# Optimization experiments

Hardware: AMD Instinct MI355X
Metric: run time of the kernel (lower is better)

Reference implementation:

```python
import jax, jax.numpy as jnp
import numpy as np

N, E = 30000, 480000
D_IN, D_HID = 128, 256
NODE_CLS, EDGE_CLS, POLAR = 5, 2, 6
EPS = 1e-5

def layer_norm(x, g, b):
    mu = jnp.mean(x, axis=-1, keepdims=True)
    var = jnp.mean((x - mu) ** 2, axis=-1, keepdims=True)
    return g * (x - mu) / jnp.sqrt(var + EPS) + b

def sage_pool(h, src, dst, Wp, bp, Ws, bs, Wn, n_nodes):
    # DGL SAGEConv aggregator_type='pool': m = relu(fc_pool(h_src)); max over in-edges
    m = jax.nn.relu(h @ Wp + bp)              # [N, d_in]
    agg = jax.ops.segment_max(m[src], dst, num_segments=n_nodes)  # [N, d_in], -inf if no in-edges
    deg = jax.ops.segment_sum(jnp.ones((src.shape[0],), jnp.float32), dst, num_segments=n_nodes)
    h_neigh = jnp.where(deg[:, None] > 0, agg, 0.0)
    out = h @ Ws + bs + h_neigh @ Wn          # fc_self + fc_neigh
    return jax.nn.relu(out)                   # activation=F.relu

def setup_inputs() -> dict:
    key = jax.random.key(0)
    ks = jax.random.split(key, 24)
    p = lambda k, shape, fan: jax.random.normal(k, shape, jnp.float32) / np.sqrt(fan)
    return {
        "h": jax.random.normal(ks[0], (N, D_IN), jnp.float32),
        "efeat": jax.random.normal(ks[1], (E, POLAR), jnp.float32),
        "src": jax.random.randint(ks[2], (E,), 0, N, jnp.int32),
        "dst": jax.random.randint(ks[3], (E,), 0, N, jnp.int32),
        # encoder SAGEConv(128->256)
        "enc_Wpool": p(ks[4], (D_IN, D_IN), D_IN), "enc_bpool": jnp.zeros((D_IN,), jnp.float32),
        "enc_Wself": p(ks[5], (D_IN, D_HID), D_IN), "enc_bself": jnp.zeros((D_HID,), jnp.float32),
        "enc_Wneigh": p(ks[6], (D_IN, D_HID), D_IN),
        # node_pred: Linear(256,5) + LayerNorm(5)
        "np_W": p(ks[7], (D_HID, NODE_CLS), D_HID), "np_b": jnp.zeros((NODE_CLS,), jnp.float32),
        "np_g": jnp.ones((NODE_CLS,), jnp.float32), "np_beta": jnp.zeros((NODE_CLS,), jnp.float32),
        # edge predictor: Linear(528,256) + LN(256) + Linear(256,2)
        "ep_W1": p(ks[8], (2 * D_HID + 2 * NODE_CLS + POLAR, D_HID), 2 * D_HID + 16),
        "ep_b1": jnp.zeros((D_HID,), jnp.float32),
        "ep_g": jnp.ones((D_HID,), jnp.float32), "ep_beta": jnp.zeros((D_HID,), jnp.float32),
        "ep_W2": p(ks[9], (D_HID, EDGE_CLS), D_HID), "ep_b2": jnp.zeros((EDGE_CLS,), jnp.float32),
        # decoder SAGEConv(256->128)
        "dec_Wpool": p(ks[10], (D_HID, D_HID), D_HID), "dec_bpool": jnp.zeros((D_HID,), jnp.float32),
        "dec_Wself": p(ks[11], (D_HID, D_IN), D_HID), "dec_bself": jnp.zeros((D_IN,), jnp.float32),
        "dec_Wneigh": p(ks[12], (D_HID, D_IN), D_HID),
    }

def reference(h, efeat, src, dst,
              enc_Wpool, enc_bpool, enc_Wself, enc_bself, enc_Wneigh,
              np_W, np_b, np_g, np_beta,
              ep_W1, ep_b1, ep_g, ep_beta, ep_W2, ep_b2,
              dec_Wpool, dec_bpool, dec_Wself, dec_bself, dec_Wneigh):
    # encoder (drop_rate == 0 path)
    h1 = sage_pool(h, src, dst, enc_Wpool, enc_bpool, enc_Wself, enc_bself, enc_Wneigh, N)
    # node head
    node_pred = layer_norm(h1 @ np_W + np_b, np_g, np_beta)  # [N, 5]
    # edge head: gather-concat-MLP per edge
    cls_sm = jax.nn.softmax(node_pred, axis=1)               # softmax once, gather per edge
    x = jnp.concatenate([h1[src], cls_sm[src], efeat, h1[dst], cls_sm[dst]], axis=1)  # [E, 528]
    x = jax.nn.relu(layer_norm(x @ ep_W1 + ep_b1, ep_g, ep_beta))
    edges_pred = x @ ep_W2 + ep_b2                           # dropout is identity in eval
    # decoder (uses original graph, input h1)
    h2 = sage_pool(h1, src, dst, dec_Wpool, dec_bpool, dec_Wself, dec_bself, dec_Wneigh, N)
    return (node_pred, edges_pred, h2)
```

## Files before the change

kernel.cpp:

```cpp
#include <hip/hip_runtime.h>

typedef unsigned short u16;
typedef unsigned int u32;
typedef __bf16 bf16_t;
typedef bf16_t bf16x8 __attribute__((ext_vector_type(8)));
typedef float f32x4 __attribute__((ext_vector_type(4)));
typedef float f32x2 __attribute__((ext_vector_type(2)));

#define N_NODES 30000
#define N_EDGES 480000

static __device__ __forceinline__ float b2f(u16 u) {
  return __uint_as_float(((u32)u) << 16);
}
static __device__ __forceinline__ float b2f_lo(u32 w) {
  return __uint_as_float(w << 16);
}
static __device__ __forceinline__ float b2f_hi(u32 w) {
  return __uint_as_float(w & 0xffff0000u);
}
static __device__ __forceinline__ u16 f2b(float f) {
  u32 x = __float_as_uint(f);
  u32 r = (x + 0x7fffu + ((x >> 16) & 1u)) >> 16;
  return (u16)r;
}

__global__ __launch_bounds__(256) void init_sniff_deg(const u16* __restrict__ h,
                                                      int* __restrict__ flag,
                                                      int* __restrict__ deg) {
  int i = blockIdx.x * 256 + threadIdx.x;
  if (i < N_NODES) deg[i] = 0;
  if (blockIdx.x == 0) {
    int t = threadIdx.x;
    int bad = 0;
#pragma unroll
    for (int j = 0; j < 4; j++) {
      u32 e = ((u32)h[t * 4 + j] >> 7) & 0xFFu;
      if (e >= 0x8Eu) bad = 1;
    }
    int r = __syncthreads_or(bad);
    if (t == 0) *flag = r ? 1 : 0;
  }
}

struct ConvDesc { const void* s; u16* d; int n; int off; };
struct ConvTab { ConvDesc e[20]; int total; };

__global__ __launch_bounds__(256) void conv_all(
    const int* __restrict__ dstE, int* __restrict__ deg,
    const void* __restrict__ hsrc, u16* __restrict__ c_h,
    const void* __restrict__ efsrc, u16* __restrict__ c_ef,
    ConvTab tab, const int* __restrict__ flag) {
  int b = blockIdx.x;
  const int t = threadIdx.x;
  if (b < 1875) {
    int e = b * 256 + t;
    if (e < N_EDGES) atomicAdd(&deg[dstE[e]], 1);
    return;
  }
  b -= 1875;
  const int f = *flag;
  if (b < 3750) {
    int i = b * 256 + t;
    if (f) {
      float4 v = ((const float4*)hsrc)[i];
      uint2 o;
      o.x = (u32)f2b(v.x) | ((u32)f2b(v.y) << 16);
      o.y = (u32)f2b(v.z) | ((u32)f2b(v.w) << 16);
      ((uint2*)c_h)[i] = o;
    } else {
      ((uint2*)c_h)[i] = ((const uint2*)hsrc)[i];
    }
    return;
  }
  b -= 3750;
  if (b < 2813) {
    int i = b * 256 + t;
    if (i < 720000) {
      if (f) {
        float4 v = ((const float4*)efsrc)[i];
        uint2 o;
        o.x = (u32)f2b(v.x) | ((u32)f2b(v.y) << 16);
        o.y = (u32)f2b(v.z) | ((u32)f2b(v.w) << 16);
        ((uint2*)c_ef)[i] = o;
      } else {
        ((uint2*)c_ef)[i] = ((const uint2*)efsrc)[i];
      }
    }
    return;
  }
  b -= 2813;
  int i = b * 256 + t;
  if (i >= tab.total) return;
#pragma unroll 1
  for (int a = 0; a < 20; a++) {
    int j = i - tab.e[a].off;
    if (j >= 0 && j < tab.e[a].n) {
      if (f) tab.e[a].d[j] = f2b(((const float*)tab.e[a].s)[j]);
      else tab.e[a].d[j] = ((const u16*)tab.e[a].s)[j];
      return;
    }
  }
}

__global__ __launch_bounds__(1024) void scan_off(const int* __restrict__ deg,
                                                 int* __restrict__ off,
                                                 int* __restrict__ cursor, int n) {
  __shared__ int carry;
  __shared__ int wsum[16];
  int t = threadIdx.x, lane = t & 63, wv = t >> 6;
  if (t == 0) { carry = 0; off[0] = 0; }
  __syncthreads();
  for (int base = 0; base < n; base += 1024) {
    int v = (base + t < n) ? deg[base + t] : 0;
    int x = v;
#pragma unroll
    for (int d = 1; d < 64; d <<= 1) {
      int y = __shfl_up(x, d, 64);
      if (lane >= d) x += y;
    }
    if (lane == 63) wsum[wv] = x;
    __syncthreads();
    int wadd = 0;
    for (int w = 0; w < wv; w++) wadd += wsum[w];
    int incl = x + wadd + carry;
    if (base + t < n) { off[base + t + 1] = incl; cursor[base + t] = incl - v; }
    __syncthreads();
    if (t == 1023) carry = incl;
    __syncthreads();
  }
}

__global__ __launch_bounds__(256) void fill_csr(const int* __restrict__ src,
                                                const int* __restrict__ dst,
                                                int* __restrict__ cursor,
                                                int* __restrict__ esrc, int nE) {
  int e = blockIdx.x * 256 + threadIdx.x;
  if (e >= nE) return;
  int p = atomicAdd(&cursor[dst[e]], 1);
  esrc[p] = src[e];
}

__global__ __launch_bounds__(256) void agg128(const u16* __restrict__ m,
                                              const int* __restrict__ esrc,
                                              const int* __restrict__ off,
                                              u16* __restrict__ out) {
  int wv = threadIdx.x >> 6, lane = threadIdx.x & 63;
  int qd = lane >> 4, l = lane & 15;
  int n = blockIdx.x * 16 + wv * 4 + qd;
  if (n >= N_NODES) return;
  int i = off[n], s1 = off[n + 1];
  u32 a0 = 0, a1 = 0, a2 = 0, a3 = 0, a4 = 0, a5 = 0, a6 = 0, a7 = 0;
  for (; i + 1 < s1; i += 2) {
    int e0 = esrc[i], e1 = esrc[i + 1];
    uint4 r0 = *(const uint4*)(m + (size_t)e0 * 128 + l * 8);
    uint4 r1 = *(const uint4*)(m + (size_t)e1 * 128 + l * 8);
    a0 = max(a0, r0.x & 0xffffu); a1 = max(a1, r0.x >> 16);
    a2 = max(a2, r0.y & 0xffffu); a3 = max(a3, r0.y >> 16);
    a4 = max(a4, r0.z & 0xffffu); a5 = max(a5, r0.z >> 16);
    a6 = max(a6, r0.w & 0xffffu); a7 = max(a7, r0.w >> 16);
    a0 = max(a0, r1.x & 0xffffu); a1 = max(a1, r1.x >> 16);
    a2 = max(a2, r1.y & 0xffffu); a3 = max(a3, r1.y >> 16);
    a4 = max(a4, r1.z & 0xffffu); a5 = max(a5, r1.z >> 16);
    a6 = max(a6, r1.w & 0xffffu); a7 = max(a7, r1.w >> 16);
  }
  if (i < s1) {
    uint4 r0 = *(const uint4*)(m + (size_t)esrc[i] * 128 + l * 8);
    a0 = max(a0, r0.x & 0xffffu); a1 = max(a1, r0.x >> 16);
    a2 = max(a2, r0.y & 0xffffu); a3 = max(a3, r0.y >> 16);
    a4 = max(a4, r0.z & 0xffffu); a5 = max(a5, r0.z >> 16);
    a6 = max(a6, r0.w & 0xffffu); a7 = max(a7, r0.w >> 16);
  }
  uint4 w;
  w.x = a0 | (a1 << 16); w.y = a2 | (a3 << 16);
  w.z = a4 | (a5 << 16); w.w = a6 | (a7 << 16);
  *(uint4*)(out + (size_t)n * 128 + l * 8) = w;
}

__global__ __launch_bounds__(256) void agg256(const u16* __restrict__ m,
                                              const int* __restrict__ esrc,
                                              const int* __restrict__ off,
                                              u16* __restrict__ out) {
  int wv = threadIdx.x >> 6, lane = threadIdx.x & 63;
  int half = lane >> 5, l = lane & 31;
  int n = blockIdx.x * 8 + wv * 2 + half;
  if (n >= N_NODES) return;
  int i = off[n], s1 = off[n + 1];
  u32 a0 = 0, a1 = 0, a2 = 0, a3 = 0, a4 = 0, a5 = 0, a6 = 0, a7 = 0;
  for (; i + 1 < s1; i += 2) {
    int e0 = esrc[i], e1 = esrc[i + 1];
    uint4 r0 = *(const uint4*)(m + (size_t)e0 * 256 + l * 8);
    uint4 r1 = *(const uint4*)(m + (size_t)e1 * 256 + l * 8);
    a0 = max(a0, r0.x & 0xffffu); a1 = max(a1, r0.x >> 16);
    a2 = max(a2, r0.y & 0xffffu); a3 = max(a3, r0.y >> 16);
    a4 = max(a4, r0.z & 0xffffu); a5 = max(a5, r0.z >> 16);
    a6 = max(a6, r0.w & 0xffffu); a7 = max(a7, r0.w >> 16);
    a0 = max(a0, r1.x & 0xffffu); a1 = max(a1, r1.x >> 16);
    a2 = max(a2, r1.y & 0xffffu); a3 = max(a3, r1.y >> 16);
    a4 = max(a4, r1.z & 0xffffu); a5 = max(a5, r1.z >> 16);
    a6 = max(a6, r1.w & 0xffffu); a7 = max(a7, r1.w >> 16);
  }
  if (i < s1) {
    uint4 r0 = *(const uint4*)(m + (size_t)esrc[i] * 256 + l * 8);
    a0 = max(a0, r0.x & 0xffffu); a1 = max(a1, r0.x >> 16);
    a2 = max(a2, r0.y & 0xffffu); a3 = max(a3, r0.y >> 16);
    a4 = max(a4, r0.z & 0xffffu); a5 = max(a5, r0.z >> 16);
    a6 = max(a6, r0.w & 0xffffu); a7 = max(a7, r0.w >> 16);
  }
  uint4 w;
  w.x = a0 | (a1 << 16); w.y = a2 | (a3 << 16);
  w.z = a4 | (a5 << 16); w.w = a6 | (a7 << 16);
  *(uint4*)(out + (size_t)n * 256 + l * 8) = w;
}

__global__ __launch_bounds__(256) void prep_weights(
    const u16* __restrict__ encWp, const u16* __restrict__ encWs, const u16* __restrict__ encWn,
    const u16* __restrict__ decWp, const u16* __restrict__ decWs, const u16* __restrict__ decWn,
    const u16* __restrict__ epW1, const u16* __restrict__ epb1,
    u16* __restrict__ wt_encpool, u16* __restrict__ wt_enc,
    u16* __restrict__ wt_decpool, u16* __restrict__ wt_dec,
    u16* __restrict__ wt_UV, u16* __restrict__ b512, float* __restrict__ swsum) {
  int b = blockIdx.x;
  const int t = threadIdx.x;
  if (b < 64) {
    int idx = b * 256 + t; int k = idx >> 7, n = idx & 127;
    wt_encpool[n * 128 + k] = encWp[k * 128 + n]; return;
  }
  b -= 64;
  if (b < 128) {
    int idx = b * 256 + t; int k = idx >> 8, n = idx & 255;
    wt_enc[n * 256 + k] = encWs[k * 256 + n]; return;
  }
  b -= 128;
  if (b < 128) {
    int idx = b * 256 + t; int k = idx >> 8, n = idx & 255;
    wt_enc[n * 256 + 128 + k] = encWn[k * 256 + n]; return;
  }
  b -= 128;
  if (b < 256) {
    int idx = b * 256 + t; int k = idx >> 8, n = idx & 255;
    wt_decpool[n * 256 + k] = decWp[k * 256 + n]; return;
  }
  b -= 256;
  if (b < 128) {
    int idx = b * 256 + t; int k = idx >> 7, n = idx & 127;
    wt_dec[n * 512 + k] = decWs[k * 128 + n]; return;
  }
  b -= 128;
  if (b < 128) {
    int idx = b * 256 + t; int k = idx >> 7, n = idx & 127;
    wt_dec[n * 512 + 256 + k] = decWn[k * 128 + n]; return;
  }
  b -= 128;
  if (b < 512) {
    int n = b, n2 = n & 255, base = (n >= 256) ? 267 : 0;
    for (int kp = t; kp < 288; kp += 256) {
      u16 v = (kp < 261) ? epW1[(size_t)(base + kp) * 256 + n2] : (u16)0;
      wt_UV[(size_t)n * 288 + kp] = v;
    }
    return;
  }
  b -= 512;
  if (b < 2) {
    int i = b * 256 + t;
    b512[i] = (i < 256) ? epb1[i] : (u16)0; return;
  }
  int k = t >> 5, l32 = t & 31;
  if (k < 6) {
    uint4 v = *(const uint4*)(epW1 + (size_t)(261 + k) * 256 + l32 * 8);
    float s = b2f_lo(v.x) + b2f_hi(v.x) + b2f_lo(v.y) + b2f_hi(v.y) +
              b2f_lo(v.z) + b2f_hi(v.z) + b2f_lo(v.w) + b2f_hi(v.w);
#pragma unroll
    for (int m = 1; m < 32; m <<= 1) s += __shfl_xor(s, m, 64);
    if (l32 == 0) swsum[k] = s;
  }
}

__global__ __launch_bounds__(256) void gemm_mfma(
    const u16* __restrict__ A0, const u16* __restrict__ A1, int K0, int K1,
    const u16* __restrict__ Bt, const u16* __restrict__ bias, int do_relu,
    u16* __restrict__ C, float* __restrict__ Cf, const int* __restrict__ flag,
    int M, int Nld) {
  __shared__ __align__(16) u16 As[128 * 40];
  __shared__ __align__(16) u16 Bs[128 * 40];
  const int t = threadIdx.x;
  const int lane = t & 63, wv = t >> 6;
  const int wm = wv & 1, wn = wv >> 1;
  const int r = lane & 15, q = lane >> 4;
  const int bm = blockIdx.x, bn = blockIdx.y;
  const int Ktot = K0 + K1;
  const bool usef = (Cf != nullptr) && (*flag != 0);

  f32x4 acc[4][4];
#pragma unroll
  for (int i = 0; i < 4; i++)
#pragma unroll
    for (int j = 0; j < 4; j++) acc[i][j] = (f32x4){0.f, 0.f, 0.f, 0.f};

  for (int kc = 0; kc < Ktot; kc += 32) {
#pragma unroll
    for (int h = 0; h < 2; h++) {
      int idx = t + h * 256;
      int rr = idx >> 2, qq = idx & 3;
      int rowg = bm * 128 + rr;
      uint4 av = make_uint4(0, 0, 0, 0);
      if (rowg < M) {
        const u16* p = (kc < K0) ? (A0 + (size_t)rowg * K0 + kc)
                                 : (A1 + (size_t)rowg * K1 + (kc - K0));
        av = *(const uint4*)(p + qq * 8);
      }
      *(uint4*)&As[rr * 40 + qq * 8] = av;
      int ng = bn * 128 + rr;
      uint4 bv = *(const uint4*)(Bt + (size_t)ng * Ktot + kc + qq * 8);
      *(uint4*)&Bs[rr * 40 + qq * 8] = bv;
    }
    __syncthreads();
    bf16x8 af[4], bfm[4];
#pragma unroll
    for (int mi = 0; mi < 4; mi++)
      af[mi] = *(const bf16x8*)&As[(wm * 64 + mi * 16 + r) * 40 + q * 8];
#pragma unroll
    for (int ni = 0; ni < 4; ni++)
      bfm[ni] = *(const bf16x8*)&Bs[(wn * 64 + ni * 16 + r) * 40 + q * 8];
#pragma unroll
    for (int mi = 0; mi < 4; mi++)
#pragma unroll
      for (int ni = 0; ni < 4; ni++)
        acc[mi][ni] = __builtin_amdgcn_mfma_f32_16x16x32_bf16(af[mi], bfm[ni], acc[mi][ni], 0, 0, 0);
    __syncthreads();
  }

  float bv[4];
#pragma unroll
  for (int ni = 0; ni < 4; ni++)
    bv[ni] = bias ? b2f(bias[bn * 128 + wn * 64 + ni * 16 + r]) : 0.f;
#pragma unroll
  for (int mi = 0; mi < 4; mi++) {
#pragma unroll
    for (int i = 0; i < 4; i++) {
      int rowg = bm * 128 + wm * 64 + mi * 16 + q * 4 + i;
      if (rowg >= M) continue;
#pragma unroll
      for (int ni = 0; ni < 4; ni++) {
        int colg = bn * 128 + wn * 64 + ni * 16 + r;
        float v = acc[mi][ni][i] + bv[ni];
        if (do_relu) v = v > 0.f ? v : 0.f;
        if (usef) Cf[(size_t)rowg * Nld + colg] = v;
        else C[(size_t)rowg * Nld + colg] = f2b(v);
      }
    }
  }
}

__global__ __launch_bounds__(256) void node_head(
    const u16* __restrict__ h1, const u16* __restrict__ W, const u16* __restrict__ b,
    const u16* __restrict__ g, const u16* __restrict__ beta,
    u16* __restrict__ outN, float* __restrict__ outNf, const int* __restrict__ flag,
    u16* __restrict__ smOut) {
  __shared__ float Wl[256 * 5];
  __shared__ float bl[5], gl[5], betal[5];
  int t = threadIdx.x;
#pragma unroll
  for (int c = 0; c < 5; c++) Wl[t * 5 + c] = b2f(W[t * 5 + c]);
  if (t < 5) { bl[t] = b2f(b[t]); gl[t] = b2f(g[t]); betal[t] = b2f(beta[t]); }
  __syncthreads();
  int n = blockIdx.x * 256 + t;
  if (n >= N_NODES) return;
  const bool usef = (*flag != 0);
  float acc[5] = {0.f, 0.f, 0.f, 0.f, 0.f};
  const u16* hp = h1 + (size_t)n * 256;
  for (int k8 = 0; k8 < 32; k8++) {
    uint4 v = *(const uint4*)(hp + k8 * 8);
    u32 wds[4] = {v.x, v.y, v.z, v.w};
#pragma unroll
    for (int h = 0; h < 4; h++) {
      float x0 = b2f_lo(wds[h]), x1 = b2f_hi(wds[h]);
      int k = k8 * 8 + h * 2;
#pragma unroll
      for (int c = 0; c < 5; c++)
        acc[c] += x0 * Wl[k * 5 + c] + x1 * Wl[(k + 1) * 5 + c];
    }
  }
  float x[5], mu = 0.f;
#pragma unroll
  for (int c = 0; c < 5; c++) { x[c] = acc[c] + bl[c]; mu += x[c]; }
  mu *= 0.2f;
  float var = 0.f;
#pragma unroll
  for (int c = 0; c < 5; c++) { float d = x[c] - mu; var += d * d; }
  var *= 0.2f;
  float rstd = rsqrtf(fmaxf(var, 0.f) + 1e-5f);
  float v5[5], mx = -1e30f;
#pragma unroll
  for (int c = 0; c < 5; c++) {
    v5[c] = gl[c] * (x[c] - mu) * rstd + betal[c];
    if (usef) outNf[(size_t)n * 5 + c] = v5[c];
    else outN[(size_t)n * 5 + c] = f2b(v5[c]);
    mx = fmaxf(mx, v5[c]);
  }
  float s = 0.f, ex[5];
#pragma unroll
  for (int c = 0; c < 5; c++) { ex[c] = __expf(v5[c] - mx); s += ex[c]; }
  float inv = 1.f / s;
  u16 row[32];
#pragma unroll
  for (int c = 0; c < 5; c++) row[c] = f2b(ex[c] * inv);
#pragma unroll
  for (int c = 5; c < 32; c++) row[c] = 0;
#pragma unroll
  for (int c = 0; c < 4; c++)
    *(uint4*)(smOut + (size_t)n * 32 + c * 8) = *(const uint4*)&row[c * 8];
}

__global__ __launch_bounds__(256) void rowsum_uv(const u16* __restrict__ UV,
                                                 float2* __restrict__ Srow) {
  int wv = threadIdx.x >> 6, lane = threadIdx.x & 63;
  int n = blockIdx.x * 4 + wv;
  if (n >= N_NODES) return;
  uint4 v = *(const uint4*)(UV + (size_t)n * 512 + lane * 8);
  float s = b2f_lo(v.x) + b2f_hi(v.x) + b2f_lo(v.y) + b2f_hi(v.y) +
            b2f_lo(v.z) + b2f_hi(v.z) + b2f_lo(v.w) + b2f_hi(v.w);
#pragma unroll
  for (int m = 1; m < 32; m <<= 1) s += __shfl_xor(s, m, 64);
  if (lane == 0) Srow[n].x = s;
  if (lane == 32) Srow[n].y = s;
}

__global__ __launch_bounds__(256) void edge_mean(
    const int* __restrict__ src, const int* __restrict__ dst,
    const u16* __restrict__ ef, const float2* __restrict__ Srow,
    const float* __restrict__ swsum, uint4* __restrict__ recs) {
  int p = blockIdx.x * 256 + threadIdx.x;
  if (p >= 240000) return;
  int e = p * 2;
  int s0 = src[e], s1 = src[e + 1];
  int d0 = dst[e], d1 = dst[e + 1];
  const u32* efp = (const u32*)(ef + (size_t)e * 6);
  u32 f0 = efp[0], f1 = efp[1], f2 = efp[2], f3 = efp[3], f4 = efp[4], f5 = efp[5];
  float xa[6] = {b2f_lo(f0), b2f_hi(f0), b2f_lo(f1), b2f_hi(f1), b2f_lo(f2), b2f_hi(f2)};
  float xb[6] = {b2f_lo(f3), b2f_hi(f3), b2f_lo(f4), b2f_hi(f4), b2f_lo(f5), b2f_hi(f5)};
  float sw[6];
#pragma unroll
  for (int k = 0; k < 6; k++) sw[k] = swsum[k];
  float m0 = Srow[s0].x + Srow[d0].y;
  float m1 = Srow[s1].x + Srow[d1].y;
#pragma unroll
  for (int k = 0; k < 6; k++) { m0 += xa[k] * sw[k]; m1 += xb[k] * sw[k]; }
  m0 *= (1.f / 256.f);
  m1 *= (1.f / 256.f);
  uint4 ra, rb, rc;
  ra.x = (u32)s0; ra.y = (u32)d0; ra.z = (u32)s1; ra.w = (u32)d1;
  rb.x = __float_as_uint(m0); rb.y = __float_as_uint(m1); rb.z = f0; rb.w = f1;
  rc.x = f2; rc.y = f3; rc.z = f4; rc.w = f5;
  recs[(size_t)p * 3 + 0] = ra;
  recs[(size_t)p * 3 + 1] = rb;
  recs[(size_t)p * 3 + 2] = rc;
}

__global__ __launch_bounds__(256) void edge_pt(
    const u16* __restrict__ UV, const uint4* __restrict__ recs,
    const u16* __restrict__ w1raw,
    const u16* __restrict__ g, const u16* __restrict__ beta,
    const u16* __restrict__ w2, const u16* __restrict__ b2,
    u16* __restrict__ outE, float* __restrict__ outEf, const int* __restrict__ flag) {
  const int t = threadIdx.x;
  const int lane = t & 63, wv = t >> 6;
  const int c0 = lane * 4;
  const int grp = (lane >> 4) & 3;
  f32x2 wefA[6], wefB[6];
#pragma unroll
  for (int k = 0; k < 6; k++) {
    u32 wa = *(const u32*)(w1raw + (size_t)(261 + k) * 256 + c0);
    u32 wb = *(const u32*)(w1raw + (size_t)(261 + k) * 256 + c0 + 2);
    wefA[k] = (f32x2){b2f_lo(wa), b2f_hi(wa)};
    wefB[k] = (f32x2){b2f_lo(wb), b2f_hi(wb)};
  }
  f32x2 glA = (f32x2){b2f(g[c0]), b2f(g[c0 + 1])};
  f32x2 glB = (f32x2){b2f(g[c0 + 2]), b2f(g[c0 + 3])};
  f32x2 blA = (f32x2){b2f(beta[c0]), b2f(beta[c0 + 1])};
  f32x2 blB = (f32x2){b2f(beta[c0 + 2]), b2f(beta[c0 + 3])};
  float w20[4], w21[4];
#pragma unroll
  for (int j = 0; j < 4; j++) {
    w20[j] = b2f(w2[(c0 + j) * 2]); w21[j] = b2f(w2[(c0 + j) * 2 + 1]);
  }
  const float b20 = b2f(b2[0]), b21 = b2f(b2[1]);
  const float bsel = (grp & 1) ? b21 : b20;
  const bool usef = (*flag != 0);
  const f32x2 zero2 = (f32x2){0.f, 0.f};

  const int pb = __builtin_amdgcn_readfirstlane((blockIdx.x * 4 + wv) * 16);
  const uint4* rp = recs + (size_t)pb * 3;
  uint4 ra = rp[0], rb = rp[1], rc = rp[2];
#pragma unroll 1
  for (int it = 0; it < 16; ++it) {
    const int e = (pb + it) * 2;
    uint4 ca = ra, cb = rb, cc = rc;
    ra = rp[3 * it + 3]; rb = rp[3 * it + 4]; rc = rp[3 * it + 5];
    const int s0 = (int)ca.x, d0 = (int)ca.y, s1 = (int)ca.z, d1 = (int)ca.w;
    const float ma = __uint_as_float(cb.x), mb = __uint_as_float(cb.y);
    float xa[6] = {b2f_lo(cb.z), b2f_hi(cb.z), b2f_lo(cb.w), b2f_hi(cb.w),
                   b2f_lo(cc.x), b2f_hi(cc.x)};
    float xb[6] = {b2f_lo(cc.y), b2f_hi(cc.y), b2f_lo(cc.z), b2f_hi(cc.z),
                   b2f_lo(cc.w), b2f_hi(cc.w)};
    uint2 ua = *(const uint2*)(UV + ((size_t)(u32)s0 << 9) + c0);
    uint2 va = *(const uint2*)(UV + ((size_t)(u32)d0 << 9) + 256 + c0);
    uint2 ub = *(const uint2*)(UV + ((size_t)(u32)s1 << 9) + c0);
    uint2 vb = *(const uint2*)(UV + ((size_t)(u32)d1 << 9) + 256 + c0);

    f32x2 yaA = (f32x2){b2f_lo(ua.x), b2f_hi(ua.x)} + (f32x2){b2f_lo(va.x), b2f_hi(va.x)};
    f32x2 yaB = (f32x2){b2f_lo(ua.y), b2f_hi(ua.y)} + (f32x2){b2f_lo(va.y), b2f_hi(va.y)};
    f32x2 ybA = (f32x2){b2f_lo(ub.x), b2f_hi(ub.x)} + (f32x2){b2f_lo(vb.x), b2f_hi(vb.x)};
    f32x2 ybB = (f32x2){b2f_lo(ub.y), b2f_hi(ub.y)} + (f32x2){b2f_lo(vb.y), b2f_hi(vb.y)};
#pragma unroll
    for (int k = 0; k < 6; k++) {
      yaA += xa[k] * wefA[k];
      yaB += xa[k] * wefB[k];
      ybA += xb[k] * wefA[k];
      ybB += xb[k] * wefB[k];
    }
    float pqa = yaA.x * yaA.x;
    pqa += yaA.y * yaA.y; pqa += yaB.x * yaB.x; pqa += yaB.y * yaB.y;
    float pqb = ybA.x * ybA.x;
    pqb += ybA.y * ybA.y; pqb += ybB.x * ybB.x; pqb += ybB.y * ybB.y;
    pqa += __shfl_xor(pqa, 32, 64);
    pqb += __shfl_xor(pqb, 32, 64);
    float z = (lane < 32) ? pqa : pqb;
#pragma unroll
    for (int m = 16; m >= 1; m >>= 1) z += __shfl_xor(z, m, 64);
    float zz = __shfl_xor(z, 32, 64);
    float pqa_t = (lane < 32) ? z : zz;
    float pqb_t = (lane < 32) ? zz : z;
    float rsa = rsqrtf(fmaxf(pqa_t * (1.f / 256.f) - ma * ma, 0.f) + 1e-5f);
    float rsb = rsqrtf(fmaxf(pqb_t * (1.f / 256.f) - mb * mb, 0.f) + 1e-5f);
    f32x2 nAa = __builtin_elementwise_max((yaA - ma) * rsa * glA + blA, zero2);
    f32x2 nAb = __builtin_elementwise_max((yaB - ma) * rsa * glB + blB, zero2);
    f32x2 nBa = __builtin_elementwise_max((ybA - mb) * rsb * glA + blA, zero2);
    f32x2 nBb = __builtin_elementwise_max((ybB - mb) * rsb * glB + blB, zero2);
    float p0a = nAa.x * w20[0], p1a = nAa.x * w21[0];
    p0a += nAa.y * w20[1]; p1a += nAa.y * w21[1];
    p0a += nAb.x * w20[2]; p1a += nAb.x * w21[2];
    p0a += nAb.y * w20[3]; p1a += nAb.y * w21[3];
    float p0b = nBa.x * w20[0], p1b = nBa.x * w21[0];
    p0b += nBa.y * w20[1]; p1b += nBa.y * w21[1];
    p0b += nBb.x * w20[2]; p1b += nBb.x * w21[2];
    p0b += nBb.y * w20[3]; p1b += nBb.y * w21[3];
    p0a += __shfl_xor(p0a, 32, 64); p1a += __shfl_xor(p1a, 32, 64);
    p0b += __shfl_xor(p0b, 32, 64); p1b += __shfl_xor(p1b, 32, 64);
    p0a += __shfl_xor(p0a, 16, 64); p1a += __shfl_xor(p1a, 16, 64);
    p0b += __shfl_xor(p0b, 16, 64); p1b += __shfl_xor(p1b, 16, 64);
    float w = (grp & 2) ? ((grp & 1) ? p1b : p0b) : ((grp & 1) ? p1a : p0a);
#pragma unroll
    for (int m = 8; m >= 1; m >>= 1) w += __shfl_xor(w, m, 64);
    if ((lane & 15) == 0) {
      float val = w + bsel;
      size_t oi = (size_t)e * 2 + grp;
      if (usef) outEf[oi] = val;
      else outE[oi] = f2b(val);
    }
  }
}

extern "C" void kernel_launch(void* const* d_in, const int* in_sizes, int n_in,
                              void* d_out, int out_size, void* d_ws, size_t ws_size,
                              hipStream_t stream) {
  char* wp = (char*)d_ws;
  auto alloc = [&](size_t bytes) -> char* {
    char* p = wp; wp += (bytes + 255) & ~(size_t)255; return p;
  };
  int* flag       = (int*)alloc(256);
  u16* c_h        = (u16*)alloc((size_t)N_NODES * 128 * 2);
  u16* c_ef       = (u16*)alloc((size_t)N_EDGES * 6 * 2);
  static const int pidx[20] = {4,5,6,7,8, 9,10,11,12, 13,14,15,16,17,18, 19,20,21,22,23};
  static const int pn[20]   = {16384,128,32768,256,32768, 1280,5,5,5,
                               135168,256,256,256,512,2, 65536,256,32768,128,32768};
  u16* cp[20];
  for (int a = 0; a < 20; a++) cp[a] = (u16*)alloc((size_t)pn[a] * 2);

  u16* wt_encpool = (u16*)alloc(128 * 128 * 2);
  u16* wt_enc     = (u16*)alloc(256 * 256 * 2);
  u16* wt_decpool = (u16*)alloc(256 * 256 * 2);
  u16* wt_dec     = (u16*)alloc(128 * 512 * 2);
  u16* wt_UV      = (u16*)alloc(512 * 288 * 2);
  u16* b512       = (u16*)alloc(512 * 2);
  float2* Srow    = (float2*)alloc((size_t)N_NODES * 8);
  float* swsum_b  = (float*)alloc(64);
  u16* m_buf      = (u16*)alloc((size_t)N_NODES * 256 * 2);
  u16* aggb       = (u16*)alloc((size_t)N_NODES * 256 * 2);
  u16* UVbuf      = m_buf;
  u16* h1b        = (u16*)alloc((size_t)N_NODES * 256 * 2);
  u16* smb32      = (u16*)alloc((size_t)N_NODES * 32 * 2);
  int* deg        = (int*)alloc((size_t)N_NODES * 4);
  int* off        = (int*)alloc((size_t)(N_NODES + 1) * 4);
  int* cursor     = (int*)alloc((size_t)N_NODES * 4);
  int* esrc       = (int*)alloc((size_t)N_EDGES * 4);
  uint4* recs     = (uint4*)alloc(((size_t)240000 * 3 + 8) * 16);

  const int* src = (const int*)d_in[2];
  const int* dst = (const int*)d_in[3];

  u16* outN = (u16*)d_out;
  u16* outE = outN + (size_t)N_NODES * 5;
  u16* outH = outN + 1110000;
  float* outNf = (float*)d_out;
  float* outEf = outNf + (size_t)N_NODES * 5;
  float* outHf = outNf + 1110000;

  init_sniff_deg<<<118, 256, 0, stream>>>((const u16*)d_in[0], flag, deg);
  ConvTab tab;
  int off_a = 0;
  for (int a = 0; a < 20; a++) {
    tab.e[a].s = d_in[pidx[a]]; tab.e[a].d = cp[a]; tab.e[a].n = pn[a]; tab.e[a].off = off_a;
    off_a += pn[a];
  }
  tab.total = off_a;
  int conv_blocks = 1875 + 3750 + 2813 + (off_a + 255) / 256;
  conv_all<<<conv_blocks, 256, 0, stream>>>(dst, deg, d_in[0], c_h, d_in[1], c_ef, tab, flag);

  const u16 *enc_Wpool = cp[0], *enc_bpool = cp[1], *enc_Wself = cp[2], *enc_bself = cp[3],
            *enc_Wneigh = cp[4], *np_W = cp[5], *np_b = cp[6], *np_g = cp[7], *np_beta = cp[8],
            *ep_W1 = cp[9], *ep_b1 = cp[10], *ep_g = cp[11], *ep_beta = cp[12],
            *ep_W2 = cp[13], *ep_b2 = cp[14], *dec_Wpool = cp[15], *dec_bpool = cp[16],
            *dec_Wself = cp[17], *dec_bself = cp[18], *dec_Wneigh = cp[19];

  scan_off<<<1, 1024, 0, stream>>>(deg, off, cursor, N_NODES);
  fill_csr<<<1875, 256, 0, stream>>>(src, dst, cursor, esrc, N_EDGES);

  prep_weights<<<1347, 256, 0, stream>>>(enc_Wpool, enc_Wself, enc_Wneigh,
                                         dec_Wpool, dec_Wself, dec_Wneigh,
                                         ep_W1, ep_b1,
                                         wt_encpool, wt_enc, wt_decpool, wt_dec,
                                         wt_UV, b512, swsum_b);

  gemm_mfma<<<dim3(235, 1), 256, 0, stream>>>(c_h, nullptr, 128, 0, wt_encpool,
                                              enc_bpool, 1, m_buf, nullptr, flag, N_NODES, 128);
  agg128<<<1875, 256, 0, stream>>>(m_buf, esrc, off, aggb);
  gemm_mfma<<<dim3(235, 2), 256, 0, stream>>>(c_h, aggb, 128, 128, wt_enc,
                                              enc_bself, 1, h1b, nullptr, flag, N_NODES, 256);
  node_head<<<118, 256, 0, stream>>>(h1b, np_W, np_b, np_g, np_beta, outN, outNf, flag, smb32);
  gemm_mfma<<<dim3(235, 4), 256, 0, stream>>>(h1b, smb32, 256, 32, wt_UV,
                                              b512, 0, UVbuf, nullptr, flag, N_NODES, 512);
  rowsum_uv<<<7500, 256, 0, stream>>>(UVbuf, Srow);
  edge_mean<<<938, 256, 0, stream>>>(src, dst, c_ef, Srow, swsum_b, recs);
  edge_pt<<<3750, 256, 0, stream>>>(UVbuf, recs, ep_W1, ep_g, ep_beta, ep_W2, ep_b2,
                                    outE, outEf, flag);
  gemm_mfma<<<dim3(235, 2), 256, 0, stream>>>(h1b, nullptr, 256, 0, wt_decpool,
                                              dec_bpool, 1, m_buf, nullptr, flag, N_NODES, 256);
  agg256<<<3750, 256, 0, stream>>>(m_buf, esrc, off, aggb);
  gemm_mfma<<<dim3(235, 1), 256, 0, stream>>>(h1b, aggb, 256, 256, wt_dec,
                                              dec_bself, 1, outH, outHf, flag, N_NODES, 128);
}
```

Before: 461.1 us.

## Software-pipeline edge UV gathers, unroll aggregation loops, and single-pass offset scan

Result: no change. 467.4 us (+1.4%).

```diff
diff --git a/kernel.cpp b/kernel.cpp
--- a/kernel.cpp
+++ b/kernel.cpp
@@ -106,28 +106,40 @@
 __global__ __launch_bounds__(1024) void scan_off(const int* __restrict__ deg,
                                                  int* __restrict__ off,
                                                  int* __restrict__ cursor, int n) {
-  __shared__ int carry;
   __shared__ int wsum[16];
-  int t = threadIdx.x, lane = t & 63, wv = t >> 6;
-  if (t == 0) { carry = 0; off[0] = 0; }
+  const int t = threadIdx.x, lane = t & 63, wv = t >> 6;
+  const int CH = 30;
+  int base = t * CH;
+  int v[CH];
+  int s = 0;
+#pragma unroll
+  for (int j = 0; j < CH; j++) {
+    int idx = base + j;
+    int d = (idx < n) ? deg[idx] : 0;
+    v[j] = s;
+    s += d;
+  }
+  int x = s;
+#pragma unroll
+  for (int d = 1; d < 64; d <<= 1) {
+    int y = __shfl_up(x, d, 64);
+    if (lane >= d) x += y;
+  }
+  if (lane == 63) wsum[wv] = x;
   __syncthreads();
-  for (int base = 0; base < n; base += 1024) {
-    int v = (base + t < n) ? deg[base + t] : 0;
-    int x = v;
-#pragma unroll
-    for (int d = 1; d < 64; d <<= 1) {
-      int y = __shfl_up(x, d, 64);
-      if (lane >= d) x += y;
-    }
-    if (lane == 63) wsum[wv] = x;
-    __syncthreads();
-    int wadd = 0;
-    for (int w = 0; w < wv; w++) wadd += wsum[w];
-    int incl = x + wadd + carry;
-    if (base + t < n) { off[base + t + 1] = incl; cursor[base + t] = incl - v; }
-    __syncthreads();
-    if (t == 1023) carry = incl;
-    __syncthreads();
+  int wadd = 0;
+  for (int w = 0; w < wv; w++) wadd += wsum[w];
+  int pref = (x - s) + wadd;
+  if (t == 0) off[0] = 0;
+#pragma unroll
+  for (int j = 0; j < CH; j++) {
+    int idx = base + j;
+    if (idx < n) {
+      int excl = pref + v[j];
+      int incl = pref + ((j + 1 < CH) ? v[j + 1] : s);
+      cursor[idx] = excl;
+      off[idx + 1] = incl;
+    }
   }
 }
 
@@ -140,6 +152,14 @@
   int p = atomicAdd(&cursor[dst[e]], 1);
   esrc[p] = src[e];
 }
+
+#define MRG(r)                                                    \
+  do {                                                            \
+    a0 = max(a0, (r).x & 0xffffu); a1 = max(a1, (r).x >> 16);     \
+    a2 = max(a2, (r).y & 0xffffu); a3 = max(a3, (r).y >> 16);     \
+    a4 = max(a4, (r).z & 0xffffu); a5 = max(a5, (r).z >> 16);     \
+    a6 = max(a6, (r).w & 0xffffu); a7 = max(a7, (r).w >> 16);     \
+  } while (0)
 
 __global__ __launch_bounds__(256) void agg128(const u16* __restrict__ m,
                                               const int* __restrict__ esrc,
@@ -151,25 +171,17 @@
   if (n >= N_NODES) return;
   int i = off[n], s1 = off[n + 1];
   u32 a0 = 0, a1 = 0, a2 = 0, a3 = 0, a4 = 0, a5 = 0, a6 = 0, a7 = 0;
-  for (; i + 1 < s1; i += 2) {
-    int e0 = esrc[i], e1 = esrc[i + 1];
+  for (; i + 3 < s1; i += 4) {
+    int e0 = esrc[i], e1 = esrc[i + 1], e2 = esrc[i + 2], e3 = esrc[i + 3];
     uint4 r0 = *(const uint4*)(m + (size_t)e0 * 128 + l * 8);
     uint4 r1 = *(const uint4*)(m + (size_t)e1 * 128 + l * 8);
-    a0 = max(a0, r0.x & 0xffffu); a1 = max(a1, r0.x >> 16);
-    a2 = max(a2, r0.y & 0xffffu); a3 = max(a3, r0.y >> 16);
-    a4 = max(a4, r0.z & 0xffffu); a5 = max(a5, r0.z >> 16);
-    a6 = max(a6, r0.w & 0xffffu); a7 = max(a7, r0.w >> 16);
-    a0 = max(a0, r1.x & 0xffffu); a1 = max(a1, r1.x >> 16);
-    a2 = max(a2, r1.y & 0xffffu); a3 = max(a3, r1.y >> 16);
-    a4 = max(a4, r1.z & 0xffffu); a5 = max(a5, r1.z >> 16);
-    a6 = max(a6, r1.w & 0xffffu); a7 = max(a7, r1.w >> 16);
-  }
-  if (i < s1) {
+    uint4 r2 = *(const uint4*)(m + (size_t)e2 * 128 + l * 8);
+    uint4 r3 = *(const uint4*)(m + (size_t)e3 * 128 + l * 8);
+    MRG(r0); MRG(r1); MRG(r2); MRG(r3);
+  }
+  for (; i < s1; i++) {
     uint4 r0 = *(const uint4*)(m + (size_t)esrc[i] * 128 + l * 8);
-    a0 = max(a0, r0.x & 0xffffu); a1 = max(a1, r0.x >> 16);
-    a2 = max(a2, r0.y & 0xffffu); a3 = max(a3, r0.y >> 16);
-    a4 = max(a4, r0.z & 0xffffu); a5 = max(a5, r0.z >> 16);
-    a6 = max(a6, r0.w & 0xffffu); a7 = max(a7, r0.w >> 16);
+    MRG(r0);
   }
   uint4 w;
   w.x = a0 | (a1 << 16); w.y = a2 | (a3 << 16);
@@ -187,31 +199,24 @@
   if (n >= N_NODES) return;
   int i = off[n], s1 = off[n + 1];
   u32 a0 = 0, a1 = 0, a2 = 0, a3 = 0, a4 = 0, a5 = 0, a6 = 0, a7 = 0;
-  for (; i + 1 < s1; i += 2) {
-    int e0 = esrc[i], e1 = esrc[i + 1];
+  for (; i + 3 < s1; i += 4) {
+    int e0 = esrc[i], e1 = esrc[i + 1], e2 = esrc[i + 2], e3 = esrc[i + 3];
     uint4 r0 = *(const uint4*)(m + (size_t)e0 * 256 + l * 8);
     uint4 r1 = *(const uint4*)(m + (size_t)e1 * 256 + l * 8);
-    a0 = max(a0, r0.x & 0xffffu); a1 = max(a1, r0.x >> 16);
-    a2 = max(a2, r0.y & 0xffffu); a3 = max(a3, r0.y >> 16);
-    a4 = max(a4, r0.z & 0xffffu); a5 = max(a5, r0.z >> 16);
-    a6 = max(a6, r0.w & 0xffffu); a7 = max(a7, r0.w >> 16);
-    a0 = max(a0, r1.x & 0xffffu); a1 = max(a1, r1.x >> 16);
-    a2 = max(a2, r1.y & 0xffffu); a3 = max(a3, r1.y >> 16);
-    a4 = max(a4, r1.z & 0xffffu); a5 = max(a5, r1.z >> 16);
-    a6 = max(a6, r1.w & 0xffffu); a7 = max(a7, r1.w >> 16);
-  }
-  if (i < s1) {
+    uint4 r2 = *(const uint4*)(m + (size_t)e2 * 256 + l * 8);
+    uint4 r3 = *(const uint4*)(m + (size_t)e3 * 256 + l * 8);
+    MRG(r0); MRG(r1); MRG(r2); MRG(r3);
+  }
+  for (; i < s1; i++) {
     uint4 r0 = *(const uint4*)(m + (size_t)esrc[i] * 256 + l * 8);
-    a0 = max(a0, r0.x & 0xffffu); a1 = max(a1, r0.x >> 16);
-    a2 = max(a2, r0.y & 0xffffu); a3 = max(a3, r0.y >> 16);
-    a4 = max(a4, r0.z & 0xffffu); a5 = max(a5, r0.z >> 16);
-    a6 = max(a6, r0.w & 0xffffu); a7 = max(a7, r0.w >> 16);
+    MRG(r0);
   }
   uint4 w;
   w.x = a0 | (a1 << 16); w.y = a2 | (a3 << 16);
   w.z = a4 | (a5 << 16); w.w = a6 | (a7 << 16);
   *(uint4*)(out + (size_t)n * 256 + l * 8) = w;
 }
+#undef MRG
 
 __global__ __launch_bounds__(256) void prep_weights(
     const u16* __restrict__ encWp, const u16* __restrict__ encWs, const u16* __restrict__ encWn,
@@ -431,7 +436,15 @@
     const u16* __restrict__ ef, const float2* __restrict__ Srow,
     const float* __restrict__ swsum, uint4* __restrict__ recs) {
   int p = blockIdx.x * 256 + threadIdx.x;
-  if (p >= 240000) return;
+  if (p >= 240000) {
+    if (p < 240016) {
+      uint4 z = make_uint4(0, 0, 0, 0);
+      recs[(size_t)p * 3 + 0] = z;
+      recs[(size_t)p * 3 + 1] = z;
+      recs[(size_t)p * 3 + 2] = z;
+    }
+    return;
+  }
   int e = p * 2;
   int s0 = src[e], s1 = src[e + 1];
   int d0 = dst[e], d1 = dst[e + 1];
@@ -491,27 +504,31 @@
 
   const int pb = __builtin_amdgcn_readfirstlane((blockIdx.x * 4 + wv) * 16);
   const uint4* rp = recs + (size_t)pb * 3;
-  uint4 ra = rp[0], rb = rp[1], rc = rp[2];
-#pragma unroll 1
+  uint4 r0a = rp[0], r0b = rp[1], r0c = rp[2];
+  uint4 r1a = rp[3], r1b = rp[4], r1c = rp[5];
+  uint2 gua = *(const uint2*)(UV + ((size_t)r0a.x << 9) + c0);
+  uint2 gva = *(const uint2*)(UV + ((size_t)r0a.y << 9) + 256 + c0);
+  uint2 gub = *(const uint2*)(UV + ((size_t)r0a.z << 9) + c0);
+  uint2 gvb = *(const uint2*)(UV + ((size_t)r0a.w << 9) + 256 + c0);
+#pragma unroll 2
   for (int it = 0; it < 16; ++it) {
     const int e = (pb + it) * 2;
-    uint4 ca = ra, cb = rb, cc = rc;
-    ra = rp[3 * it + 3]; rb = rp[3 * it + 4]; rc = rp[3 * it + 5];
-    const int s0 = (int)ca.x, d0 = (int)ca.y, s1 = (int)ca.z, d1 = (int)ca.w;
-    const float ma = __uint_as_float(cb.x), mb = __uint_as_float(cb.y);
-    float xa[6] = {b2f_lo(cb.z), b2f_hi(cb.z), b2f_lo(cb.w), b2f_hi(cb.w),
-                   b2f_lo(cc.x), b2f_hi(cc.x)};
-    float xb[6] = {b2f_lo(cc.y), b2f_hi(cc.y), b2f_lo(cc.z), b2f_hi(cc.z),
-                   b2f_lo(cc.w), b2f_hi(cc.w)};
-    uint2 ua = *(const uint2*)(UV + ((size_t)(u32)s0 << 9) + c0);
-    uint2 va = *(const uint2*)(UV + ((size_t)(u32)d0 << 9) + 256 + c0);
-    uint2 ub = *(const uint2*)(UV + ((size_t)(u32)s1 << 9) + c0);
-    uint2 vb = *(const uint2*)(UV + ((size_t)(u32)d1 << 9) + 256 + c0);
-
-    f32x2 yaA = (f32x2){b2f_lo(ua.x), b2f_hi(ua.x)} + (f32x2){b2f_lo(va.x), b2f_hi(va.x)};
-    f32x2 yaB = (f32x2){b2f_lo(ua.y), b2f_hi(ua.y)} + (f32x2){b2f_lo(va.y), b2f_hi(va.y)};
-    f32x2 ybA = (f32x2){b2f_lo(ub.x), b2f_hi(ub.x)} + (f32x2){b2f_lo(vb.x), b2f_hi(vb.x)};
-    f32x2 ybB = (f32x2){b2f_lo(ub.y), b2f_hi(ub.y)} + (f32x2){b2f_lo(vb.y), b2f_hi(vb.y)};
+    uint2 hua = *(const uint2*)(UV + ((size_t)r1a.x << 9) + c0);
+    uint2 hva = *(const uint2*)(UV + ((size_t)r1a.y << 9) + 256 + c0);
+    uint2 hub = *(const uint2*)(UV + ((size_t)r1a.z << 9) + c0);
+    uint2 hvb = *(const uint2*)(UV + ((size_t)r1a.w << 9) + 256 + c0);
+    uint4 r2a = rp[3 * it + 6], r2b = rp[3 * it + 7], r2c = rp[3 * it + 8];
+
+    const float ma = __uint_as_float(r0b.x), mb = __uint_as_float(r0b.y);
+    float xa[6] = {b2f_lo(r0b.z), b2f_hi(r0b.z), b2f_lo(r0b.w), b2f_hi(r0b.w),
+                   b2f_lo(r0c.x), b2f_hi(r0c.x)};
+    float xb[6] = {b2f_lo(r0c.y), b2f_hi(r0c.y), b2f_lo(r0c.z), b2f_hi(r0c.z),
+                   b2f_lo(r0c.w), b2f_hi(r0c.w)};
+
+    f32x2 yaA = (f32x2){b2f_lo(gua.x), b2f_hi(gua.x)} + (f32x2){b2f_lo(gva.x), b2f_hi(gva.x)};
+    f32x2 yaB = (f32x2){b2f_lo(gua.y), b2f_hi(gua.y)} + (f32x2){b2f_lo(gva.y), b2f_hi(gva.y)};
+    f32x2 ybA = (f32x2){b2f_lo(gub.x), b2f_hi(gub.x)} + (f32x2){b2f_lo(gvb.x), b2f_hi(gvb.x)};
+    f32x2 ybB = (f32x2){b2f_lo(gub.y), b2f_hi(gub.y)} + (f32x2){b2f_lo(gvb.y), b2f_hi(gvb.y)};
 #pragma unroll
     for (int k = 0; k < 6; k++) {
       yaA += xa[k] * wefA[k];
@@ -558,6 +575,9 @@
       if (usef) outEf[oi] = val;
       else outE[oi] = f2b(val);
     }
+    r0a = r1a; r0b = r1b; r0c = r1c;
+    r1a = r2a; r1b = r2b; r1c = r2c;
+    gua = hua; gva = hva; gub = hub; gvb = hvb;
   }
 }
 
@@ -594,7 +614,7 @@
   int* off        = (int*)alloc((size_t)(N_NODES + 1) * 4);
   int* cursor     = (int*)alloc((size_t)N_NODES * 4);
   int* esrc       = (int*)alloc((size_t)N_EDGES * 4);
-  uint4* recs     = (uint4*)alloc(((size_t)240000 * 3 + 8) * 16);
+  uint4* recs     = (uint4*)alloc(((size_t)240000 * 3 + 64) * 16);
 
   const int* src = (const int*)d_in[2];
   const int* dst = (const int*)d_in[3];
```

## Process edge MLP per destination node using CSR order to reuse V rows

Applied to the files above, without the earlier changes.

New measurement: 477.2 us. 1.03x slower.

```diff
diff --git a/kernel.cpp b/kernel.cpp
--- a/kernel.cpp
+++ b/kernel.cpp
@@ -134,12 +134,22 @@
 __global__ __launch_bounds__(256) void fill_csr(const int* __restrict__ src,
                                                 const int* __restrict__ dst,
                                                 int* __restrict__ cursor,
-                                                int* __restrict__ esrc, int nE) {
+                                                int* __restrict__ esrc,
+                                                int* __restrict__ epos, int nE) {
   int e = blockIdx.x * 256 + threadIdx.x;
   if (e >= nE) return;
   int p = atomicAdd(&cursor[dst[e]], 1);
   esrc[p] = src[e];
-}
+  epos[e] = p;
+}
+
+#define MRG(r)                                                    \
+  do {                                                            \
+    a0 = max(a0, (r).x & 0xffffu); a1 = max(a1, (r).x >> 16);     \
+    a2 = max(a2, (r).y & 0xffffu); a3 = max(a3, (r).y >> 16);     \
+    a4 = max(a4, (r).z & 0xffffu); a5 = max(a5, (r).z >> 16);     \
+    a6 = max(a6, (r).w & 0xffffu); a7 = max(a7, (r).w >> 16);     \
+  } while (0)
 
 __global__ __launch_bounds__(256) void agg128(const u16* __restrict__ m,
                                               const int* __restrict__ esrc,
@@ -155,21 +165,11 @@
     int e0 = esrc[i], e1 = esrc[i + 1];
     uint4 r0 = *(const uint4*)(m + (size_t)e0 * 128 + l * 8);
     uint4 r1 = *(const uint4*)(m + (size_t)e1 * 128 + l * 8);
-    a0 = max(a0, r0.x & 0xffffu); a1 = max(a1, r0.x >> 16);
-    a2 = max(a2, r0.y & 0xffffu); a3 = max(a3, r0.y >> 16);
-    a4 = max(a4, r0.z & 0xffffu); a5 = max(a5, r0.z >> 16);
-    a6 = max(a6, r0.w & 0xffffu); a7 = max(a7, r0.w >> 16);
-    a0 = max(a0, r1.x & 0xffffu); a1 = max(a1, r1.x >> 16);
-    a2 = max(a2, r1.y & 0xffffu); a3 = max(a3, r1.y >> 16);
-    a4 = max(a4, r1.z & 0xffffu); a5 = max(a5, r1.z >> 16);
-    a6 = max(a6, r1.w & 0xffffu); a7 = max(a7, r1.w >> 16);
+    MRG(r0); MRG(r1);
   }
   if (i < s1) {
     uint4 r0 = *(const uint4*)(m + (size_t)esrc[i] * 128 + l * 8);
-    a0 = max(a0, r0.x & 0xffffu); a1 = max(a1, r0.x >> 16);
-    a2 = max(a2, r0.y & 0xffffu); a3 = max(a3, r0.y >> 16);
-    a4 = max(a4, r0.z & 0xffffu); a5 = max(a5, r0.z >> 16);
-    a6 = max(a6, r0.w & 0xffffu); a7 = max(a7, r0.w >> 16);
+    MRG(r0);
   }
   uint4 w;
   w.x = a0 | (a1 << 16); w.y = a2 | (a3 << 16);
@@ -191,27 +191,18 @@
     int e0 = esrc[i], e1 = esrc[i + 1];
     uint4 r0 = *(const uint4*)(m + (size_t)e0 * 256 + l * 8);
     uint4 r1 = *(const uint4*)(m + (size_t)e1 * 256 + l * 8);
-    a0 = max(a0, r0.x & 0xffffu); a1 = max(a1, r0.x >> 16);
-    a2 = max(a2, r0.y & 0xffffu); a3 = max(a3, r0.y >> 16);
-    a4 = max(a4, r0.z & 0xffffu); a5 = max(a5, r0.z >> 16);
-    a6 = max(a6, r0.w & 0xffffu); a7 = max(a7, r0.w >> 16);
-    a0 = max(a0, r1.x & 0xffffu); a1 = max(a1, r1.x >> 16);
-    a2 = max(a2, r1.y & 0xffffu); a3 = max(a3, r1.y >> 16);
-    a4 = max(a4, r1.z & 0xffffu); a5 = max(a5, r1.z >> 16);
-    a6 = max(a6, r1.w & 0xffffu); a7 = max(a7, r1.w >> 16);
+    MRG(r0); MRG(r1);
   }
   if (i < s1) {
     uint4 r0 = *(const uint4*)(m + (size_t)esrc[i] * 256 + l * 8);
-    a0 = max(a0, r0.x & 0xffffu); a1 = max(a1, r0.x >> 16);
-    a2 = max(a2, r0.y & 0xffffu); a3 = max(a3, r0.y >> 16);
-    a4 = max(a4, r0.z & 0xffffu); a5 = max(a5, r0.z >> 16);
-    a6 = max(a6, r0.w & 0xffffu); a7 = max(a7, r0.w >> 16);
+    MRG(r0);
   }
   uint4 w;
   w.x = a0 | (a1 << 16); w.y = a2 | (a3 << 16);
   w.z = a4 | (a5 << 16); w.w = a6 | (a7 << 16);
   *(uint4*)(out + (size_t)n * 256 + l * 8) = w;
 }
+#undef MRG
 
 __global__ __launch_bounds__(256) void prep_weights(
     const u16* __restrict__ encWp, const u16* __restrict__ encWs, const u16* __restrict__ encWn,
@@ -429,42 +420,38 @@
 __global__ __launch_bounds__(256) void edge_mean(
     const int* __restrict__ src, const int* __restrict__ dst,
     const u16* __restrict__ ef, const float2* __restrict__ Srow,
-    const float* __restrict__ swsum, uint4* __restrict__ recs) {
-  int p = blockIdx.x * 256 + threadIdx.x;
-  if (p >= 240000) return;
-  int e = p * 2;
-  int s0 = src[e], s1 = src[e + 1];
-  int d0 = dst[e], d1 = dst[e + 1];
+    const float* __restrict__ swsum, const int* __restrict__ epos,
+    uint4* __restrict__ recs) {
+  int e = blockIdx.x * 256 + threadIdx.x;
+  if (e >= N_EDGES) return;
+  int s0 = src[e], d0 = dst[e];
   const u32* efp = (const u32*)(ef + (size_t)e * 6);
-  u32 f0 = efp[0], f1 = efp[1], f2 = efp[2], f3 = efp[3], f4 = efp[4], f5 = efp[5];
+  u32 f0 = efp[0], f1 = efp[1], f2 = efp[2];
   float xa[6] = {b2f_lo(f0), b2f_hi(f0), b2f_lo(f1), b2f_hi(f1), b2f_lo(f2), b2f_hi(f2)};
-  float xb[6] = {b2f_lo(f3), b2f_hi(f3), b2f_lo(f4), b2f_hi(f4), b2f_lo(f5), b2f_hi(f5)};
   float sw[6];
 #pragma unroll
   for (int k = 0; k < 6; k++) sw[k] = swsum[k];
   float m0 = Srow[s0].x + Srow[d0].y;
-  float m1 = Srow[s1].x + Srow[d1].y;
-#pragma unroll
-  for (int k = 0; k < 6; k++) { m0 += xa[k] * sw[k]; m1 += xb[k] * sw[k]; }
+#pragma unroll
+  for (int k = 0; k < 6; k++) m0 += xa[k] * sw[k];
   m0 *= (1.f / 256.f);
-  m1 *= (1.f / 256.f);
-  uint4 ra, rb, rc;
-  ra.x = (u32)s0; ra.y = (u32)d0; ra.z = (u32)s1; ra.w = (u32)d1;
-  rb.x = __float_as_uint(m0); rb.y = __float_as_uint(m1); rb.z = f0; rb.w = f1;
-  rc.x = f2; rc.y = f3; rc.z = f4; rc.w = f5;
-  recs[(size_t)p * 3 + 0] = ra;
-  recs[(size_t)p * 3 + 1] = rb;
-  recs[(size_t)p * 3 + 2] = rc;
+  int p = epos[e];
+  uint4 r0, r1;
+  r0.x = (u32)s0; r0.y = (u32)e; r0.z = __float_as_uint(m0); r0.w = f0;
+  r1.x = f1; r1.y = f2; r1.z = 0; r1.w = 0;
+  recs[(size_t)p * 2 + 0] = r0;
+  recs[(size_t)p * 2 + 1] = r1;
 }
 
 __global__ __launch_bounds__(256) void edge_pt(
     const u16* __restrict__ UV, const uint4* __restrict__ recs,
+    const int* __restrict__ off,
     const u16* __restrict__ w1raw,
     const u16* __restrict__ g, const u16* __restrict__ beta,
     const u16* __restrict__ w2, const u16* __restrict__ b2,
     u16* __restrict__ outE, float* __restrict__ outEf, const int* __restrict__ flag) {
   const int t = threadIdx.x;
-  const int lane = t & 63, wv = t >> 6;
+  const int lane = t & 63;
   const int c0 = lane * 4;
   const int grp = (lane >> 4) & 3;
   f32x2 wefA[6], wefB[6];
@@ -489,29 +476,34 @@
   const bool usef = (*flag != 0);
   const f32x2 zero2 = (f32x2){0.f, 0.f};
 
-  const int pb = __builtin_amdgcn_readfirstlane((blockIdx.x * 4 + wv) * 16);
-  const uint4* rp = recs + (size_t)pb * 3;
-  uint4 ra = rp[0], rb = rp[1], rc = rp[2];
-#pragma unroll 1
-  for (int it = 0; it < 16; ++it) {
-    const int e = (pb + it) * 2;
-    uint4 ca = ra, cb = rb, cc = rc;
-    ra = rp[3 * it + 3]; rb = rp[3 * it + 4]; rc = rp[3 * it + 5];
-    const int s0 = (int)ca.x, d0 = (int)ca.y, s1 = (int)ca.z, d1 = (int)ca.w;
-    const float ma = __uint_as_float(cb.x), mb = __uint_as_float(cb.y);
-    float xa[6] = {b2f_lo(cb.z), b2f_hi(cb.z), b2f_lo(cb.w), b2f_hi(cb.w),
-                   b2f_lo(cc.x), b2f_hi(cc.x)};
-    float xb[6] = {b2f_lo(cc.y), b2f_hi(cc.y), b2f_lo(cc.z), b2f_hi(cc.z),
-                   b2f_lo(cc.w), b2f_hi(cc.w)};
-    uint2 ua = *(const uint2*)(UV + ((size_t)(u32)s0 << 9) + c0);
-    uint2 va = *(const uint2*)(UV + ((size_t)(u32)d0 << 9) + 256 + c0);
-    uint2 ub = *(const uint2*)(UV + ((size_t)(u32)s1 << 9) + c0);
-    uint2 vb = *(const uint2*)(UV + ((size_t)(u32)d1 << 9) + 256 + c0);
-
-    f32x2 yaA = (f32x2){b2f_lo(ua.x), b2f_hi(ua.x)} + (f32x2){b2f_lo(va.x), b2f_hi(va.x)};
-    f32x2 yaB = (f32x2){b2f_lo(ua.y), b2f_hi(ua.y)} + (f32x2){b2f_lo(va.y), b2f_hi(va.y)};
-    f32x2 ybA = (f32x2){b2f_lo(ub.x), b2f_hi(ub.x)} + (f32x2){b2f_lo(vb.x), b2f_hi(vb.x)};
-    f32x2 ybB = (f32x2){b2f_lo(ub.y), b2f_hi(ub.y)} + (f32x2){b2f_lo(vb.y), b2f_hi(vb.y)};
+  const int n = __builtin_amdgcn_readfirstlane(blockIdx.x * 4 + (t >> 6));
+  if (n >= N_NODES) return;
+  int i = __builtin_amdgcn_readfirstlane(off[n]);
+  const int s1 = __builtin_amdgcn_readfirstlane(off[n + 1]);
+  if (i >= s1) return;
+  uint2 vn = *(const uint2*)(UV + ((size_t)(u32)n << 9) + 256 + c0);
+  const f32x2 vA = (f32x2){b2f_lo(vn.x), b2f_hi(vn.x)};
+  const f32x2 vB = (f32x2){b2f_lo(vn.y), b2f_hi(vn.y)};
+
+  for (; i < s1; i += 2) {
+    const bool two = (i + 1 < s1);
+    const int ib = two ? i + 1 : i;
+    uint4 ra0 = recs[(size_t)i * 2], ra1 = recs[(size_t)i * 2 + 1];
+    uint4 rb0 = recs[(size_t)ib * 2], rb1 = recs[(size_t)ib * 2 + 1];
+    const int sa = (int)ra0.x, ea = (int)ra0.y;
+    const int sb = (int)rb0.x, eb = (int)rb0.y;
+    const float ma = __uint_as_float(ra0.z), mb = __uint_as_float(rb0.z);
+    float xa[6] = {b2f_lo(ra0.w), b2f_hi(ra0.w), b2f_lo(ra1.x), b2f_hi(ra1.x),
+                   b2f_lo(ra1.y), b2f_hi(ra1.y)};
+    float xb[6] = {b2f_lo(rb0.w), b2f_hi(rb0.w), b2f_lo(rb1.x), b2f_hi(rb1.x),
+                   b2f_lo(rb1.y), b2f_hi(rb1.y)};
+    uint2 ua = *(const uint2*)(UV + ((size_t)(u32)sa << 9) + c0);
+    uint2 ub = *(const uint2*)(UV + ((size_t)(u32)sb << 9) + c0);
+
+    f32x2 yaA = (f32x2){b2f_lo(ua.x), b2f_hi(ua.x)} + vA;
+    f32x2 yaB = (f32x2){b2f_lo(ua.y), b2f_hi(ua.y)} + vB;
+    f32x2 ybA = (f32x2){b2f_lo(ub.x), b2f_hi(ub.x)} + vA;
+    f32x2 ybB = (f32x2){b2f_lo(ub.y), b2f_hi(ub.y)} + vB;
 #pragma unroll
     for (int k = 0; k < 6; k++) {
       yaA += xa[k] * wefA[k];
@@ -554,9 +546,15 @@
     for (int m = 8; m >= 1; m >>= 1) w += __shfl_xor(w, m, 64);
     if ((lane & 15) == 0) {
       float val = w + bsel;
-      size_t oi = (size_t)e * 2 + grp;
-      if (usef) outEf[oi] = val;
-      else outE[oi] = f2b(val);
+      if (grp & 2) {
+        if (two) {
+          size_t oi = (size_t)eb * 2 + (grp & 1);
+          if (usef) outEf[oi] = val; else outE[oi] = f2b(val);
+        }
+      } else {
+        size_t oi = (size_t)ea * 2 + (grp & 1);
+        if (usef) outEf[oi] = val; else outE[oi] = f2b(val);
+      }
     }
   }
 }
@@ -594,7 +592,8 @@
   int* off        = (int*)alloc((size_t)(N_NODES + 1) * 4);
   int* cursor     = (int*)alloc((size_t)N_NODES * 4);
   int* esrc       = (int*)alloc((size_t)N_EDGES * 4);
-  uint4* recs     = (uint4*)alloc(((size_t)240000 * 3 + 8) * 16);
+  int* epos       = (int*)alloc((size_t)N_EDGES * 4);
+  uint4* recs     = (uint4*)alloc(((size_t)N_EDGES * 2 + 8) * 16);
 
   const int* src = (const int*)d_in[2];
   const int* dst = (const int*)d_in[3];
@@ -624,7 +623,7 @@
             *dec_Wself = cp[17], *dec_bself = cp[18], *dec_Wneigh = cp[19];
 
   scan_off<<<1, 1024, 0, stream>>>(deg, off, cursor, N_NODES);
-  fill_csr<<<1875, 256, 0, stream>>>(src, dst, cursor, esrc, N_EDGES);
+  fill_csr<<<1875, 256, 0, stream>>>(src, dst, cursor, esrc, epos, N_EDGES);
 
   prep_weights<<<1347, 256, 0, stream>>>(enc_Wpool, enc_Wself, enc_Wneigh,
                                          dec_Wpool, dec_Wself, dec_Wneigh,
@@ -641,8 +640,8 @@
   gemm_mfma<<<dim3(235, 4), 256, 0, stream>>>(h1b, smb32, 256, 32, wt_UV,
                                               b512, 0, UVbuf, nullptr, flag, N_NODES, 512);
   rowsum_uv<<<7500, 256, 0, stream>>>(UVbuf, Srow);
-  edge_mean<<<938, 256, 0, stream>>>(src, dst, c_ef, Srow, swsum_b, recs);
-  edge_pt<<<3750, 256, 0, stream>>>(UVbuf, recs, ep_W1, ep_g, ep_beta, ep_W2, ep_b2,
+  edge_mean<<<1875, 256, 0, stream>>>(src, dst, c_ef, Srow, swsum_b, epos, recs);
+  edge_pt<<<7500, 256, 0, stream>>>(UVbuf, recs, off, ep_W1, ep_g, ep_beta, ep_W2, ep_b2,
                                     outE, outEf, flag);
   gemm_mfma<<<dim3(235, 2), 256, 0, stream>>>(h1b, nullptr, 256, 0, wt_decpool,
                                               dec_bpool, 1, m_buf, nullptr, flag, N_NODES, 256);
```
